# Kernel optimization log

Hardware: AMD Instinct MI355X
Metric: run time of the kernel (lower is better)

The kernel has to match this reference:

```python
import jax, jax.numpy as jnp
import numpy as np

B, S, D = 2, 2048, 2048
N_HEADS, N_KV_HEADS = 16, 4
HEAD_DIM = D // N_HEADS  # 128
THETA = 10000.0
NEG_INF = -1e9


def setup_inputs() -> dict:
    key = jax.random.key(0)
    k1, k2, k3 = jax.random.split(key, 3)
    x = jax.random.normal(k1, (B, S, D), dtype=jnp.float32)
    w_qkv = jax.random.normal(k2, ((N_HEADS + 2 * N_KV_HEADS) * HEAD_DIM, D), dtype=jnp.float32) * (D ** -0.5)
    w_o = jax.random.normal(k3, (D, N_HEADS * HEAD_DIM), dtype=jnp.float32) * (D ** -0.5)
    return {"x": x, "w_qkv": w_qkv, "w_o": w_o}


def _apply_rope(q, k, seq_len, theta):
    # q: [B,S,Hq,hd], k: [B,S,Hk,hd]
    hd = q.shape[-1]
    t = jnp.arange(seq_len, dtype=jnp.float32)
    inv_freq = 1.0 / (theta ** (jnp.arange(0, hd, 2, dtype=jnp.float32) / hd))
    freqs = jnp.outer(t, inv_freq)            # [S, hd/2]
    cos = jnp.cos(freqs)[:, None, :]          # [S,1,hd/2] broadcasts over B,H
    sin = jnp.sin(freqs)[:, None, :]

    def rot(v):
        b, s, h, _ = v.shape
        v2 = v.reshape(b, s, h, hd // 2, 2)
        v0, v1 = v2[..., 0], v2[..., 1]
        out = jnp.stack([v0 * cos - v1 * sin, v0 * sin + v1 * cos], axis=-1)
        return out.reshape(b, s, h, hd)

    return rot(q), rot(k)


def reference(x, w_qkv, w_o):
    b, s, _ = x.shape
    q_size = N_HEADS * HEAD_DIM
    kv_size = N_KV_HEADS * HEAD_DIM
    # fused QKV projection
    qkv = jnp.einsum('bsd,od->bso', x, w_qkv)
    q = qkv[:, :, :q_size].reshape(b, s, N_HEADS, HEAD_DIM)
    k = qkv[:, :, q_size:q_size + kv_size].reshape(b, s, N_KV_HEADS, HEAD_DIM)
    v = qkv[:, :, q_size + kv_size:].reshape(b, s, N_KV_HEADS, HEAD_DIM)
    # RoPE
    q, k = _apply_rope(q, k, s, THETA)
    # GQA: repeat kv heads (repeat_interleave along head dim)
    rep = N_HEADS // N_KV_HEADS
    k = jnp.repeat(k, rep, axis=2)
    v = jnp.repeat(v, rep, axis=2)
    # [B,H,S,hd]
    q = q.transpose(0, 2, 1, 3)
    k = k.transpose(0, 2, 1, 3)
    v = v.transpose(0, 2, 1, 3)
    scale = HEAD_DIM ** -0.5
    scores = jnp.einsum('bhqd,bhkd->bhqk', q, k) * scale
    causal = jnp.tril(jnp.ones((s, s), dtype=bool))
    scores = jnp.where(causal[None, None], scores, NEG_INF)
    attn = jax.nn.softmax(scores, axis=-1)
    out = jnp.einsum('bhqk,bhkd->bhqd', attn, v)
    out = out.transpose(0, 2, 1, 3).reshape(b, s, N_HEADS * HEAD_DIM)
    return jnp.einsum('bsd,od->bso', out, w_o)
```

## Files before the change

kernel.cpp:

```cpp
#include <hip/hip_runtime.h>
#include <hip/hip_bf16.h>
#include <cstdint>
#include <cstddef>

typedef float f32x4 __attribute__((ext_vector_type(4)));
typedef float f32x16 __attribute__((ext_vector_type(16)));
typedef __bf16 bf16x8 __attribute__((ext_vector_type(8)));
typedef unsigned short us8v __attribute__((ext_vector_type(8)));
typedef unsigned short us4v __attribute__((ext_vector_type(4)));

constexpr int B_ = 2, S_ = 2048, D_ = 2048, NH = 16, NKV = 4, HD = 128;
constexpr int QKV_O = (NH + 2 * NKV) * HD;

__device__ __forceinline__ unsigned short f2b(float f) {
  union { float f; uint32_t u; } v{f};
  uint32_t r = v.u + 0x7fffu + ((v.u >> 16) & 1u);
  return (unsigned short)(r >> 16);
}

__device__ __forceinline__ uint32_t pk2(float a, float b) {
  union { __bf16 h[2]; uint32_t u; } v;
  v.h[0] = (__bf16)a; v.h[1] = (__bf16)b;
  return v.u;
}

__device__ __forceinline__ bf16x8 as_bf(us8v x) {
  union { us8v u; bf16x8 b; } v; v.u = x; return v.b;
}

__device__ __forceinline__ f32x4 mfma16(bf16x8 a, bf16x8 b, f32x4 c) {
  return __builtin_amdgcn_mfma_f32_16x16x32_bf16(a, b, c, 0, 0, 0);
}
__device__ __forceinline__ f32x16 mfma32(bf16x8 a, bf16x8 b, f32x16 c) {
  return __builtin_amdgcn_mfma_f32_32x32x16_bf16(a, b, c, 0, 0, 0);
}

__device__ __forceinline__ void gload_lds16(const unsigned short* g, unsigned short* l) {
  __builtin_amdgcn_global_load_lds(
      (const __attribute__((address_space(1))) unsigned int*)(uintptr_t)g,
      (__attribute__((address_space(3))) unsigned int*)(uintptr_t)l, 16, 0, 0);
}

__global__ void f2b_kernel(const float* __restrict__ in, unsigned short* __restrict__ out, int n4) {
  int i = blockIdx.x * blockDim.x + threadIdx.x;
  if (i >= n4) return;
  float4 v = reinterpret_cast<const float4*>(in)[i];
  us4v o;
  o[0] = f2b(v.x); o[1] = f2b(v.y); o[2] = f2b(v.z); o[3] = f2b(v.w);
  reinterpret_cast<us4v*>(out)[i] = o;
}

__global__ void rope_table_kernel(float* __restrict__ cs, float* __restrict__ sn) {
  int idx = blockIdx.x * blockDim.x + threadIdx.x;
  if (idx >= S_ * 64) return;
  int t = idx >> 6, i = idx & 63;
  float inv = __expf(-((float)(2 * i) / 128.0f) * 9.210340371976184f);
  float fr = (float)t * inv;
  cs[idx] = cosf(fr);
  sn[idx] = sinf(fr);
}

__global__ void rope_qk_kernel(const float* __restrict__ qkv, const float* __restrict__ cs,
                               const float* __restrict__ sn, unsigned short* __restrict__ Q,
                               unsigned short* __restrict__ K2) {
  int idx = blockIdx.x * blockDim.x + threadIdx.x;
  if (idx >= B_ * S_ * 20 * 64) return;
  int pr = idx & 63;
  int tmp = idx >> 6;
  int hh = tmp % 20; tmp /= 20;
  int s = tmp % S_;
  int b = tmp / S_;
  int off = (hh < 16) ? hh * HD : NH * HD + (hh - 16) * HD;
  float2 v = *reinterpret_cast<const float2*>(qkv + (size_t)(b * S_ + s) * QKV_O + off + 2 * pr);
  float c0 = cs[s * 64 + pr], s0 = sn[s * 64 + pr];
  float mult = (hh < 16) ? 0.12751744f : 1.0f;
  float o0 = (v.x * c0 - v.y * s0) * mult;
  float o1 = (v.x * s0 + v.y * c0) * mult;
  unsigned int packed = (unsigned)f2b(o0) | ((unsigned)f2b(o1) << 16);
  if (hh < 16) {
    *reinterpret_cast<unsigned*>(Q + (((size_t)(b * NH + hh) * S_ + s) * HD + 2 * pr)) = packed;
  } else {
    int bk = b * NKV + (hh - 16);
    size_t a = (((size_t)bk * 16 + (pr >> 2)) * S_ + s) * 8 + (pr & 3) * 2;
    *reinterpret_cast<unsigned*>(K2 + a) = packed;
  }
}

__global__ __launch_bounds__(128) void v8_kernel(const float* __restrict__ qkv,
                                                 unsigned short* __restrict__ V2) {
  int d = threadIdx.x;
  int g = blockIdx.x;
  int bk = blockIdx.y;
  const float* src = qkv + (size_t)((bk >> 2) * S_ + g * 8) * QKV_O + (NH + NKV) * HD +
                     (bk & 3) * HD + d;
  us8v o;
#pragma unroll
  for (int j = 0; j < 8; j++) o[j] = f2b(src[(size_t)j * QKV_O]);
  *reinterpret_cast<us8v*>(V2 + (((size_t)bk * 256 + g) * 128 + d) * 8) = o;
}

__global__ __launch_bounds__(256) void gemm_bt_kernel(const unsigned short* __restrict__ A,
                                                      const unsigned short* __restrict__ Bm,
                                                      float* __restrict__ C, int M, int N, int K) {
  __shared__ unsigned short As[128 * 32];
  __shared__ unsigned short Bs[128 * 32];
  int t = threadIdx.x;
  int lane = t & 63, wid = t >> 6;
  int wr = wid >> 1, wc = wid & 1;
  int g = lane >> 4, c = lane & 15;
  int m0 = blockIdx.y * 128, n0 = blockIdx.x * 128;

  int r0 = wid * 32 + (lane >> 2);
  int cc = (lane & 3) * 8;
  const unsigned short* pa = A + (size_t)(m0 + r0) * K + cc;
  const unsigned short* pb = Bm + (size_t)(n0 + r0) * K + cc;
  unsigned short* lA = As + wid * 1024;
  unsigned short* lB = Bs + wid * 1024;

  f32x4 acc[4][4] = {};
  for (int k0 = 0; k0 < K; k0 += 32) {
    gload_lds16(pa + k0, lA);
    gload_lds16(pa + (size_t)16 * K + k0, lA + 512);
    gload_lds16(pb + k0, lB);
    gload_lds16(pb + (size_t)16 * K + k0, lB + 512);
    __syncthreads();
    bf16x8 af[4], bfv[4];
#pragma unroll
    for (int m = 0; m < 4; m++)
      af[m] = as_bf(*reinterpret_cast<const us8v*>(&As[(wr * 64 + m * 16 + c) * 32 + g * 8]));
#pragma unroll
    for (int n = 0; n < 4; n++)
      bfv[n] = as_bf(*reinterpret_cast<const us8v*>(&Bs[(wc * 64 + n * 16 + c) * 32 + g * 8]));
#pragma unroll
    for (int m = 0; m < 4; m++)
#pragma unroll
      for (int n = 0; n < 4; n++) acc[m][n] = mfma16(af[m], bfv[n], acc[m][n]);
    __syncthreads();
  }
#pragma unroll
  for (int m = 0; m < 4; m++)
#pragma unroll
    for (int n = 0; n < 4; n++)
#pragma unroll
      for (int r = 0; r < 4; r++)
        C[(size_t)(m0 + wr * 64 + m * 16 + g * 4 + r) * N + n0 + wc * 64 + n * 16 + c] =
            acc[m][n][r];
}

__global__ __launch_bounds__(512, 2) void gemm8p_kernel(const unsigned short* __restrict__ A,
                                                        const unsigned short* __restrict__ Bm,
                                                        float* __restrict__ C, int M, int N,
                                                        int K) {
  __shared__ unsigned short LDS[65536];
  const int t = threadIdx.x;
  const int lane = t & 63, wid = t >> 6;
  const int wm = wid >> 2, wn = wid & 3;
  const int c = lane & 15, g4 = lane >> 4;
  const int m0 = blockIdx.y * 256, n0 = blockIdx.x * 256;

  const int sr = t >> 3, ss = t & 7;
  const int sg = ss ^ (sr & 7);
  const unsigned short* pa = A + (size_t)(m0 + sr) * K + sg * 8;
  const unsigned short* pb = Bm + (size_t)(n0 + sr) * K + sg * 8;
  unsigned short* ldw = (unsigned short*)&LDS[wid << 9];

  f32x4 acc[8][4] = {};
  bf16x8 bf[4][2];

#define STAGE_A(buf, j, kk0) \
  gload_lds16(pa + (size_t)(64 * (j)) * K + (kk0), ldw + (buf)*16384 + (j)*4096)
#define STAGE_B(buf, j, kk0) \
  gload_lds16(pb + (size_t)(64 * (j)) * K + (kk0), ldw + 32768 + (buf)*16384 + (j)*4096)

#define LDA(buf, m, kk) \
  as_bf(*reinterpret_cast<const us8v*>( \
      &LDS[(buf)*16384 + (wm * 128 + (m)*16 + c) * 64 + ((((kk) << 2) | g4) ^ (c & 7)) * 8]))
#define LDB(buf, n, kk) \
  as_bf(*reinterpret_cast<const us8v*>( \
      &LDS[32768 + (buf)*16384 + (wn * 64 + (n)*16 + c) * 64 + ((((kk) << 2) | g4) ^ (c & 7)) * 8]))

#pragma unroll
  for (int j = 0; j < 4; j++) STAGE_B(0, j, 0);
#pragma unroll
  for (int j = 0; j < 4; j++) STAGE_A(0, j, 0);
  asm volatile("s_waitcnt vmcnt(0)" ::: "memory");
  __builtin_amdgcn_s_barrier();

  const int NT = K >> 6;
  for (int tt = 0; tt < NT; ++tt) {
    const int cur = tt & 1, nxt = cur ^ 1;
    const int kn = (tt + 1) << 6;
    const bool st = (tt + 1) < NT;
    bf16x8 a00, a01, a10, a11;

#define MFMA_PAIR(mlo)                                    \
  __builtin_amdgcn_s_setprio(1);                          \
  _Pragma("unroll") for (int n = 0; n < 4; n++) {         \
    acc[(mlo)][n] = mfma16(a00, bf[n][0], acc[(mlo)][n]); \
    acc[(mlo) + 1][n] = mfma16(a10, bf[n][0], acc[(mlo) + 1][n]); \
    acc[(mlo)][n] = mfma16(a01, bf[n][1], acc[(mlo)][n]); \
    acc[(mlo) + 1][n] = mfma16(a11, bf[n][1], acc[(mlo) + 1][n]); \
  }                                                       \
  __builtin_amdgcn_s_setprio(0);

#pragma unroll
    for (int n = 0; n < 4; n++) { bf[n][0] = LDB(cur, n, 0); bf[n][1] = LDB(cur, n, 1); }
    a00 = LDA(cur, 0, 0); a01 = LDA(cur, 0, 1); a10 = LDA(cur, 1, 0); a11 = LDA(cur, 1, 1);
    if (st) { STAGE_B(nxt, 0, kn); STAGE_B(nxt, 1, kn); }
    __builtin_amdgcn_s_barrier();
    MFMA_PAIR(0)
    __builtin_amdgcn_s_barrier();
    a00 = LDA(cur, 2, 0); a01 = LDA(cur, 2, 1); a10 = LDA(cur, 3, 0); a11 = LDA(cur, 3, 1);
    if (st) { STAGE_B(nxt, 2, kn); STAGE_B(nxt, 3, kn); }
    asm volatile("s_waitcnt vmcnt(4)" ::: "memory");
    __builtin_amdgcn_s_barrier();
    MFMA_PAIR(2)
    __builtin_amdgcn_s_barrier();
    a00 = LDA(cur, 4, 0); a01 = LDA(cur, 4, 1); a10 = LDA(cur, 5, 0); a11 = LDA(cur, 5, 1);
    if (st) { STAGE_A(nxt, 0, kn); STAGE_A(nxt, 2, kn); }
    __builtin_amdgcn_s_barrier();
    MFMA_PAIR(4)
    __builtin_amdgcn_s_barrier();
    a00 = LDA(cur, 6, 0); a01 = LDA(cur, 6, 1); a10 = LDA(cur, 7, 0); a11 = LDA(cur, 7, 1);
    if (st) { STAGE_A(nxt, 1, kn); STAGE_A(nxt, 3, kn); }
    asm volatile("s_waitcnt vmcnt(2)" ::: "memory");
    __builtin_amdgcn_s_barrier();
    MFMA_PAIR(6)
    __builtin_amdgcn_s_barrier();
#undef MFMA_PAIR
  }

#pragma unroll
  for (int m = 0; m < 8; m++)
#pragma unroll
    for (int n = 0; n < 4; n++)
#pragma unroll
      for (int r = 0; r < 4; r++)
        C[(size_t)(m0 + wm * 128 + m * 16 + g4 * 4 + r) * N + n0 + wn * 64 + n * 16 + c] =
            acc[m][n][r];
#undef STAGE_A
#undef STAGE_B
#undef LDA
#undef LDB
}

__global__ __launch_bounds__(256, 2) void attn32_kernel(const unsigned short* __restrict__ Q,
                                                        const unsigned short* __restrict__ K2,
                                                        const unsigned short* __restrict__ V2,
                                                        unsigned short* __restrict__ O) {
  int t = threadIdx.x;
  int lane = t & 63, wid = t >> 6;
  int l31 = lane & 31, hi = lane >> 5;

  int id = blockIdx.x;
  int g = id & 7, s5 = id >> 3;
  int b = g >> 2, kvh = g & 3;
  int h = kvh * 4 + (s5 & 3);
  int bk = b * NKV + kvh;
  int pidx = (s5 >> 2) * 2 + (wid >> 1);
  int tw = (wid & 1) ? (63 - pidx) : pidx;
  int qw = tw * 32;

  const unsigned short* Qp = Q + ((size_t)(b * NH + h) * S_ + qw) * HD + (size_t)l31 * HD + hi * 8;
  const unsigned short* Kp = K2 + (((size_t)bk * 16 + hi) * S_ + l31) * 8;
  const unsigned short* Vp = V2 + (((size_t)bk * 256 + hi) * 128 + l31) * 8;

  bf16x8 qf[8];
#pragma unroll
  for (int kk = 0; kk < 8; kk++)
    qf[kk] = as_bf(*reinterpret_cast<const us8v*>(Qp + kk * 16));

  f32x16 oacc[4] = {};
  float mrow = -1e30f, lsum = 0.0f;

  bf16x8 kA[8], kB[8];

  auto loadK = [&](bf16x8(&kf)[8], int kv) {
    const unsigned short* kp = Kp + (size_t)kv * 8;
#pragma unroll
    for (int kk = 0; kk < 8; kk++)
      kf[kk] = as_bf(*reinterpret_cast<const us8v*>(kp + (size_t)kk * 2 * S_ * 8));
  };

  auto step = [&](bf16x8(&kf)[8], bf16x8(&kn)[8], int kv0) {
    bf16x8 vf[8];
    const unsigned short* vp = Vp + (size_t)kv0 * 128;
#pragma unroll
    for (int dt = 0; dt < 4; dt++) {
      vf[2 * dt] = as_bf(*reinterpret_cast<const us8v*>(vp + dt * 256));
      vf[2 * dt + 1] = as_bf(*reinterpret_cast<const us8v*>(vp + 2048 + dt * 256));
    }
    if (kv0 + 32 <= qw) loadK(kn, kv0 + 32);

    f32x16 sa = {}, sb = {};
    __builtin_amdgcn_s_setprio(1);
#pragma unroll
    for (int kk = 0; kk < 4; kk++) {
      sa = mfma32(kf[2 * kk], qf[2 * kk], sa);
      sb = mfma32(kf[2 * kk + 1], qf[2 * kk + 1], sb);
    }
    __builtin_amdgcn_s_setprio(0);
    f32x16 s = sa + sb;

    if (kv0 == qw) {
      int qg = qw + l31;
#pragma unroll
      for (int r = 0; r < 16; r++) {
        int kvg = kv0 + (r & 3) + 8 * (r >> 2) + 4 * hi;
        if (kvg > qg) s[r] = -1e30f;
      }
    }

    float pm = fmaxf(s[0], s[1]);
#pragma unroll
    for (int r = 2; r < 16; r++) pm = fmaxf(pm, s[r]);
    pm = fmaxf(pm, __shfl_xor(pm, 32));

    bool nore = __all(pm <= mrow + 11.54f) != 0;
    float mn = nore ? mrow : fmaxf(mrow, pm);
    float part = 0.0f;
    uint32_t w[8];
#pragma unroll
    for (int jj = 0; jj < 8; jj++) {
      float e0 = __builtin_amdgcn_exp2f(s[2 * jj] - mn);
      float e1 = __builtin_amdgcn_exp2f(s[2 * jj + 1] - mn);
      part += e0 + e1;
      w[jj] = pk2(e0, e1);
    }
    part += __shfl_xor(part, 32);
    if (nore) {
      lsum += part;
    } else {
      float alpha = __builtin_amdgcn_exp2f(mrow - mn);
      lsum = lsum * alpha + part;
      mrow = mn;
#pragma unroll
      for (int r = 0; r < 16; r++) {
        float af = __shfl(alpha, (r & 3) + 8 * (r >> 2) + 4 * hi);
#pragma unroll
        for (int dt = 0; dt < 4; dt++) oacc[dt][r] *= af;
      }
    }

    uint32_t sw[8];
#pragma unroll
    for (int jj = 0; jj < 8; jj++) sw[jj] = __shfl_xor(w[jj], 32);
    union { uint32_t u[4]; bf16x8 v; } pa0, pa1;
    if (hi == 0) {
      pa0.u[0] = w[0]; pa0.u[1] = w[1]; pa0.u[2] = sw[0]; pa0.u[3] = sw[1];
      pa1.u[0] = w[4]; pa1.u[1] = w[5]; pa1.u[2] = sw[4]; pa1.u[3] = sw[5];
    } else {
      pa0.u[0] = sw[2]; pa0.u[1] = sw[3]; pa0.u[2] = w[2]; pa0.u[3] = w[3];
      pa1.u[0] = sw[6]; pa1.u[1] = sw[7]; pa1.u[2] = w[6]; pa1.u[3] = w[7];
    }

    __builtin_amdgcn_s_setprio(1);
#pragma unroll
    for (int dt = 0; dt < 4; dt++) {
      oacc[dt] = mfma32(pa0.v, vf[2 * dt], oacc[dt]);
      oacc[dt] = mfma32(pa1.v, vf[2 * dt + 1], oacc[dt]);
    }
    __builtin_amdgcn_s_setprio(0);
  };

  loadK(kA, 0);
  int kv0 = 0;
  while (true) {
    step(kA, kB, kv0);
    kv0 += 32;
    if (kv0 > qw) break;
    step(kB, kA, kv0);
    kv0 += 32;
    if (kv0 > qw) break;
  }

  float il = 1.0f / lsum;
  unsigned short* Op = O + ((size_t)b * S_ + qw) * D_ + h * HD;
#pragma unroll
  for (int r = 0; r < 16; r++) {
    int row = (r & 3) + 8 * (r >> 2) + 4 * hi;
    float sc = __shfl(il, row);
#pragma unroll
    for (int dt = 0; dt < 4; dt++)
      Op[(size_t)row * D_ + dt * 32 + l31] = f2b(oacc[dt][r] * sc);
  }
}

extern "C" void kernel_launch(void* const* d_in, const int* in_sizes, int n_in, void* d_out,
                              int out_size, void* d_ws, size_t ws_size, hipStream_t stream) {
  const float* x = (const float*)d_in[0];
  const float* w_qkv = (const float*)d_in[1];
  const float* w_o = (const float*)d_in[2];
  float* out = (float*)d_out;

  char* ws = (char*)d_ws;
  size_t off = 0;
  auto alloc = [&](size_t bytes) -> void* {
    void* p = ws + off;
    off += (bytes + 255) & ~(size_t)255;
    return p;
  };
  const size_t nx = (size_t)B_ * S_ * D_;
  const size_t nwqkv = (size_t)QKV_O * D_;
  const size_t nwo = (size_t)D_ * D_;
  unsigned short* xb = (unsigned short*)alloc(nx * 2);
  unsigned short* wqkvb = (unsigned short*)alloc(nwqkv * 2);
  unsigned short* wob = (unsigned short*)alloc(nwo * 2);
  float* qkv = (float*)alloc((size_t)B_ * S_ * QKV_O * 4);
  unsigned short* Qb = (unsigned short*)alloc((size_t)B_ * NH * S_ * HD * 2);
  unsigned short* K2b = (unsigned short*)alloc((size_t)B_ * NKV * S_ * HD * 2);
  unsigned short* V2b = (unsigned short*)alloc((size_t)B_ * NKV * HD * S_ * 2);
  unsigned short* attnb = (unsigned short*)alloc((size_t)B_ * S_ * D_ * 2);
  float* cs = (float*)alloc((size_t)S_ * 64 * 4);
  float* sn = (float*)alloc((size_t)S_ * 64 * 4);

  f2b_kernel<<<dim3((nx / 4 + 255) / 256), 256, 0, stream>>>(x, xb, nx / 4);
  f2b_kernel<<<dim3((nwqkv / 4 + 255) / 256), 256, 0, stream>>>(w_qkv, wqkvb, nwqkv / 4);
  f2b_kernel<<<dim3((nwo / 4 + 255) / 256), 256, 0, stream>>>(w_o, wob, nwo / 4);
  rope_table_kernel<<<dim3((S_ * 64 + 255) / 256), 256, 0, stream>>>(cs, sn);

  gemm8p_kernel<<<dim3(QKV_O / 256, (B_ * S_) / 256), 512, 0, stream>>>(xb, wqkvb, qkv,
                                                                        B_ * S_, QKV_O, D_);

  rope_qk_kernel<<<dim3((B_ * S_ * 20 * 64 + 255) / 256), 256, 0, stream>>>(qkv, cs, sn, Qb, K2b);
  v8_kernel<<<dim3(S_ / 8, B_ * NKV), 128, 0, stream>>>(qkv, V2b);

  attn32_kernel<<<dim3(512), 256, 0, stream>>>(Qb, K2b, V2b, attnb);

  gemm_bt_kernel<<<dim3(D_ / 128, (B_ * S_) / 128), 256, 0, stream>>>(attnb, wob, out,
                                                                      B_ * S_, D_, D_);
}
```

Before: 220.7 us.

## Replace output projection GEMM with pipelined 256x128 kernel and XCD-aware block remap

Swaps the simple single-buffered 128x128 output-projection GEMM for a new double-buffered, LDS-swizzled 256x128 variant of the pipelined QKV GEMM, which interleaves its staging loads with MFMA work. Both GEMMs now launch on a 1D grid whose block IDs are remapped so that consecutive tiles go to the same XCD, aiming for better L2 reuse. The goal is to cut global-load latency stalls and raise MFMA utilisation in the output projection. The cost is larger LDS use per block and a remap that assumes the grid size divides by 8.

```diff
diff --git a/kernel.cpp b/kernel.cpp
--- a/kernel.cpp
+++ b/kernel.cpp
@@ -99,64 +99,18 @@
   *reinterpret_cast<us8v*>(V2 + (((size_t)bk * 256 + g) * 128 + d) * 8) = o;
 }
 
-__global__ __launch_bounds__(256) void gemm_bt_kernel(const unsigned short* __restrict__ A,
-                                                      const unsigned short* __restrict__ Bm,
-                                                      float* __restrict__ C, int M, int N, int K) {
-  __shared__ unsigned short As[128 * 32];
-  __shared__ unsigned short Bs[128 * 32];
-  int t = threadIdx.x;
-  int lane = t & 63, wid = t >> 6;
-  int wr = wid >> 1, wc = wid & 1;
-  int g = lane >> 4, c = lane & 15;
-  int m0 = blockIdx.y * 128, n0 = blockIdx.x * 128;
-
-  int r0 = wid * 32 + (lane >> 2);
-  int cc = (lane & 3) * 8;
-  const unsigned short* pa = A + (size_t)(m0 + r0) * K + cc;
-  const unsigned short* pb = Bm + (size_t)(n0 + r0) * K + cc;
-  unsigned short* lA = As + wid * 1024;
-  unsigned short* lB = Bs + wid * 1024;
-
-  f32x4 acc[4][4] = {};
-  for (int k0 = 0; k0 < K; k0 += 32) {
-    gload_lds16(pa + k0, lA);
-    gload_lds16(pa + (size_t)16 * K + k0, lA + 512);
-    gload_lds16(pb + k0, lB);
-    gload_lds16(pb + (size_t)16 * K + k0, lB + 512);
-    __syncthreads();
-    bf16x8 af[4], bfv[4];
-#pragma unroll
-    for (int m = 0; m < 4; m++)
-      af[m] = as_bf(*reinterpret_cast<const us8v*>(&As[(wr * 64 + m * 16 + c) * 32 + g * 8]));
-#pragma unroll
-    for (int n = 0; n < 4; n++)
-      bfv[n] = as_bf(*reinterpret_cast<const us8v*>(&Bs[(wc * 64 + n * 16 + c) * 32 + g * 8]));
-#pragma unroll
-    for (int m = 0; m < 4; m++)
-#pragma unroll
-      for (int n = 0; n < 4; n++) acc[m][n] = mfma16(af[m], bfv[n], acc[m][n]);
-    __syncthreads();
-  }
-#pragma unroll
-  for (int m = 0; m < 4; m++)
-#pragma unroll
-    for (int n = 0; n < 4; n++)
-#pragma unroll
-      for (int r = 0; r < 4; r++)
-        C[(size_t)(m0 + wr * 64 + m * 16 + g * 4 + r) * N + n0 + wc * 64 + n * 16 + c] =
-            acc[m][n][r];
-}
-
 __global__ __launch_bounds__(512, 2) void gemm8p_kernel(const unsigned short* __restrict__ A,
                                                         const unsigned short* __restrict__ Bm,
                                                         float* __restrict__ C, int M, int N,
-                                                        int K) {
+                                                        int K, int nbx) {
   __shared__ unsigned short LDS[65536];
   const int t = threadIdx.x;
   const int lane = t & 63, wid = t >> 6;
   const int wm = wid >> 2, wn = wid & 3;
   const int c = lane & 15, g4 = lane >> 4;
-  const int m0 = blockIdx.y * 256, n0 = blockIdx.x * 256;
+  const int cpx = gridDim.x >> 3;
+  const int nid = (blockIdx.x & 7) * cpx + (blockIdx.x >> 3);
+  const int m0 = (nid / nbx) * 256, n0 = (nid % nbx) * 256;
 
   const int sr = t >> 3, ss = t & 7;
   const int sg = ss ^ (sr & 7);
@@ -237,6 +191,104 @@
 #pragma unroll
       for (int r = 0; r < 4; r++)
         C[(size_t)(m0 + wm * 128 + m * 16 + g4 * 4 + r) * N + n0 + wn * 64 + n * 16 + c] =
+            acc[m][n][r];
+#undef STAGE_A
+#undef STAGE_B
+#undef LDA
+#undef LDB
+}
+
+__global__ __launch_bounds__(512, 2) void gemm8pn_kernel(const unsigned short* __restrict__ A,
+                                                         const unsigned short* __restrict__ Bm,
+                                                         float* __restrict__ C, int M, int N,
+                                                         int K, int nbx) {
+  __shared__ unsigned short LDS[49152];
+  const int t = threadIdx.x;
+  const int lane = t & 63, wid = t >> 6;
+  const int wm = wid >> 2, wn = wid & 3;
+  const int c = lane & 15, g4 = lane >> 4;
+  const int cpx = gridDim.x >> 3;
+  const int nid = (blockIdx.x & 7) * cpx + (blockIdx.x >> 3);
+  const int m0 = (nid / nbx) * 256, n0 = (nid % nbx) * 128;
+
+  const int sr = t >> 3, ss = t & 7;
+  const int sg = ss ^ (sr & 7);
+  const unsigned short* pa = A + (size_t)(m0 + sr) * K + sg * 8;
+  const unsigned short* pb = Bm + (size_t)(n0 + sr) * K + sg * 8;
+  unsigned short* ldw = (unsigned short*)&LDS[wid << 9];
+
+  f32x4 acc[8][2] = {};
+  bf16x8 bf[2][2];
+
+#define STAGE_A(buf, j, kk0) \
+  gload_lds16(pa + (size_t)(64 * (j)) * K + (kk0), ldw + (buf)*16384 + (j)*4096)
+#define STAGE_B(buf, j, kk0) \
+  gload_lds16(pb + (size_t)(64 * (j)) * K + (kk0), ldw + 32768 + (buf)*8192 + (j)*4096)
+
+#define LDA(buf, m, kk) \
+  as_bf(*reinterpret_cast<const us8v*>( \
+      &LDS[(buf)*16384 + (wm * 128 + (m)*16 + c) * 64 + ((((kk) << 2) | g4) ^ (c & 7)) * 8]))
+#define LDB(buf, n, kk) \
+  as_bf(*reinterpret_cast<const us8v*>( \
+      &LDS[32768 + (buf)*8192 + (wn * 32 + (n)*16 + c) * 64 + ((((kk) << 2) | g4) ^ (c & 7)) * 8]))
+
+  STAGE_B(0, 0, 0); STAGE_B(0, 1, 0);
+#pragma unroll
+  for (int j = 0; j < 4; j++) STAGE_A(0, j, 0);
+  asm volatile("s_waitcnt vmcnt(0)" ::: "memory");
+  __builtin_amdgcn_s_barrier();
+
+  const int NT = K >> 6;
+  for (int tt = 0; tt < NT; ++tt) {
+    const int cur = tt & 1, nxt = cur ^ 1;
+    const int kn = (tt + 1) << 6;
+    const bool st = (tt + 1) < NT;
+    bf16x8 a00, a01, a10, a11;
+
+#define MFMA_PAIR(mlo)                                    \
+  __builtin_amdgcn_s_setprio(1);                          \
+  _Pragma("unroll") for (int n = 0; n < 2; n++) {         \
+    acc[(mlo)][n] = mfma16(a00, bf[n][0], acc[(mlo)][n]); \
+    acc[(mlo) + 1][n] = mfma16(a10, bf[n][0], acc[(mlo) + 1][n]); \
+    acc[(mlo)][n] = mfma16(a01, bf[n][1], acc[(mlo)][n]); \
+    acc[(mlo) + 1][n] = mfma16(a11, bf[n][1], acc[(mlo) + 1][n]); \
+  }                                                       \
+  __builtin_amdgcn_s_setprio(0);
+
+#pragma unroll
+    for (int n = 0; n < 2; n++) { bf[n][0] = LDB(cur, n, 0); bf[n][1] = LDB(cur, n, 1); }
+    a00 = LDA(cur, 0, 0); a01 = LDA(cur, 0, 1); a10 = LDA(cur, 1, 0); a11 = LDA(cur, 1, 1);
+    if (st) STAGE_B(nxt, 0, kn);
+    __builtin_amdgcn_s_barrier();
+    MFMA_PAIR(0)
+    __builtin_amdgcn_s_barrier();
+    a00 = LDA(cur, 2, 0); a01 = LDA(cur, 2, 1); a10 = LDA(cur, 3, 0); a11 = LDA(cur, 3, 1);
+    if (st) STAGE_B(nxt, 1, kn);
+    asm volatile("s_waitcnt vmcnt(2)" ::: "memory");
+    __builtin_amdgcn_s_barrier();
+    MFMA_PAIR(2)
+    __builtin_amdgcn_s_barrier();
+    a00 = LDA(cur, 4, 0); a01 = LDA(cur, 4, 1); a10 = LDA(cur, 5, 0); a11 = LDA(cur, 5, 1);
+    if (st) { STAGE_A(nxt, 0, kn); STAGE_A(nxt, 2, kn); }
+    __builtin_amdgcn_s_barrier();
+    MFMA_PAIR(4)
+    __builtin_amdgcn_s_barrier();
+    a00 = LDA(cur, 6, 0); a01 = LDA(cur, 6, 1); a10 = LDA(cur, 7, 0); a11 = LDA(cur, 7, 1);
+    if (st) { STAGE_A(nxt, 1, kn); STAGE_A(nxt, 3, kn); }
+    asm volatile("s_waitcnt vmcnt(2)" ::: "memory");
+    __builtin_amdgcn_s_barrier();
+    MFMA_PAIR(6)
+    __builtin_amdgcn_s_barrier();
+#undef MFMA_PAIR
+  }
+
+#pragma unroll
+  for (int m = 0; m < 8; m++)
+#pragma unroll
+    for (int n = 0; n < 2; n++)
+#pragma unroll
+      for (int r = 0; r < 4; r++)
+        C[(size_t)(m0 + wm * 128 + m * 16 + g4 * 4 + r) * N + n0 + wn * 32 + n * 16 + c] =
             acc[m][n][r];
 #undef STAGE_A
 #undef STAGE_B
@@ -419,14 +471,12 @@
   f2b_kernel<<<dim3((nwo / 4 + 255) / 256), 256, 0, stream>>>(w_o, wob, nwo / 4);
   rope_table_kernel<<<dim3((S_ * 64 + 255) / 256), 256, 0, stream>>>(cs, sn);
 
-  gemm8p_kernel<<<dim3(QKV_O / 256, (B_ * S_) / 256), 512, 0, stream>>>(xb, wqkvb, qkv,
-                                                                        B_ * S_, QKV_O, D_);
+  gemm8p_kernel<<<dim3(192), 512, 0, stream>>>(xb, wqkvb, qkv, B_ * S_, QKV_O, D_, QKV_O / 256);
 
   rope_qk_kernel<<<dim3((B_ * S_ * 20 * 64 + 255) / 256), 256, 0, stream>>>(qkv, cs, sn, Qb, K2b);
   v8_kernel<<<dim3(S_ / 8, B_ * NKV), 128, 0, stream>>>(qkv, V2b);
 
   attn32_kernel<<<dim3(512), 256, 0, stream>>>(Qb, K2b, V2b, attnb);
 
-  gemm_bt_kernel<<<dim3(D_ / 128, (B_ * S_) / 128), 256, 0, stream>>>(attnb, wob, out,
-                                                                      B_ * S_, D_, D_);
-}
+  gemm8pn_kernel<<<dim3(256), 512, 0, stream>>>(attnb, wob, out, B_ * S_, D_, D_, D_ / 128);
+}
```

Result: faster. 210.5 us (-4.6%).
